# Performance work log

Hardware: AMD Instinct MI355X
Metric: run time of the kernel (lower is better)

The kernel has to match this reference:

```python
import jax, jax.numpy as jnp
import numpy as np
import math

B, S, D, H, L, K = 4, 2048, 256, 8, 2, 3  # batch, seq, dim, heads, MTA layers, conv kernel
HS = D // H
EPS = 1e-6


def layer_norm(x, g, b):
    m = jnp.mean(x, axis=-1, keepdims=True)
    v = jnp.mean((x - m) ** 2, axis=-1, keepdims=True)
    return (x - m) * jax.lax.rsqrt(v + EPS) * g + b


def temporal_encoder(x, W, b):
    # x: [B,S,D]; W: [L,K,D,D] (WIO), b: [L,D]. Stack of kernel-3 'SAME' Conv1d, GELU between.
    for i in range(L):
        x = jax.lax.conv_general_dilated(
            x, W[i], window_strides=(1,), padding=[(1, 1)],
            dimension_numbers=("NWC", "WIO", "NWC")) + b[i]
        if i < L - 1:
            x = jax.nn.gelu(x)
    return x


def setup_inputs() -> dict:
    key = jax.random.key(0)
    ks = jax.random.split(key, 10)
    w = lambda k, shape: jax.random.normal(k, shape, jnp.float32) * 0.02
    return {
        "x": jax.random.normal(ks[0], (B, S, D), jnp.float32),
        "ln1_g": jnp.ones((D,), jnp.float32), "ln1_b": jnp.zeros((D,), jnp.float32),
        "Wq": w(ks[1], (L, K, D, D)), "bq": jnp.zeros((L, D), jnp.float32),
        "Wk": w(ks[2], (L, K, D, D)), "bk": jnp.zeros((L, D), jnp.float32),
        "Wv": w(ks[3], (L, K, D, D)), "bv": jnp.zeros((L, D), jnp.float32),
        "ln2_g": jnp.ones((D,), jnp.float32), "ln2_b": jnp.zeros((D,), jnp.float32),
        "Wo1": w(ks[4], (D, D)), "bo1": jnp.zeros((D,), jnp.float32),
        "Wo2": w(ks[5], (D, D)), "bo2": jnp.zeros((D,), jnp.float32),
        "mask": jax.random.randint(ks[6], (B, S), 0, 2).astype(jnp.int32),
    }


def reference(x, ln1_g, ln1_b, Wq, bq, Wk, bk, Wv, bv, ln2_g, ln2_b, Wo1, bo1, Wo2, bo2, mask):
    b_, s_ = x.shape[0], x.shape[1]
    h = layer_norm(x, ln1_g, ln1_b)
    q = temporal_encoder(h, Wq, bq).reshape(b_, s_, H, HS)
    k = temporal_encoder(h, Wk, bk).reshape(b_, s_, H, HS)
    v = temporal_encoder(h, Wv, bv).reshape(b_, s_, H, HS)
    # attention scores [B,H,S,S]
    scores = jnp.einsum("bqhd,bkhd->bhqk", q, k) / math.sqrt(HS)
    m = mask[:, None, None, :].astype(scores.dtype)  # [B,1,1,S]
    scores = scores + (1.0 - m) * (-1e30)
    probs = jax.nn.softmax(scores, axis=-1)
    attn = jnp.einsum("bhqk,bkhd->bqhd", probs, v).reshape(b_, s_, D)
    residual = x + attn  # dropout p=0
    o = layer_norm(residual, ln2_g, ln2_b)
    o = jax.nn.gelu(o @ Wo1 + bo1)  # 1x1 Conv1D == per-token linear
    o = o @ Wo2 + bo2 + residual
    return o
```

## Files before the change

### kernel.cpp

```cpp
#include <hip/hip_runtime.h>
#include <hip/hip_bf16.h>
#include <math.h>

#define BB 4
#define SS 2048
#define DD 256
#define HH 8
#define HSZ 32

typedef __attribute__((ext_vector_type(8))) short short8;
typedef __attribute__((ext_vector_type(4))) float f32x4;

__device__ __forceinline__ void gload_lds16(const void* g, void* l) {
    __builtin_amdgcn_global_load_lds((const unsigned int*)g, (unsigned int*)l,
                                     16, 0, 0);
}

__device__ __forceinline__ float exp2_hw(float x) {
    float r;
    asm("v_exp_f32 %0, %1" : "=v"(r) : "v"(x));
    return r;
}

__device__ __forceinline__ unsigned int perm_pack(float a, float b, unsigned int sel) {
    unsigned int r;
    asm("v_perm_b32 %0, %1, %2, %3"
        : "=v"(r)
        : "v"(__float_as_uint(b)), "v"(__float_as_uint(a)), "s"(sel));
    return r;
}

__device__ __forceinline__ float gelu_f(float x) {
    float x3 = x * x * x;
    float z = 0.7978845608028654f * fmaf(0.044715f, x3, x);
    float e = __expf(2.0f * z);
    float t = 1.0f - 2.0f / (e + 1.0f);
    return 0.5f * x * (1.0f + t);
}

__device__ __forceinline__ unsigned short f2bf(float f) {
    unsigned int u = __float_as_uint(f);
    u = (u + 0x7fffu + ((u >> 16) & 1u)) >> 16;
    return (unsigned short)u;
}

template<bool HASRES>
__device__ __forceinline__ void ln_wave_body(
    int t, int lane,
    const float* __restrict__ x, const float* __restrict__ addin,
    const float* __restrict__ g, const float* __restrict__ bvec,
    float* __restrict__ resid_out, unsigned short* __restrict__ oln_bf)
{
    const int base = t * DD + lane * 4;
    float4 v4 = *(const float4*)&x[base];
    if (HASRES) {
        float4 a4 = *(const float4*)&addin[base];
        v4.x += a4.x; v4.y += a4.y; v4.z += a4.z; v4.w += a4.w;
        *(float4*)&resid_out[base] = v4;
    }
    float s = (v4.x + v4.y) + (v4.z + v4.w);
    #pragma unroll
    for (int o = 1; o < 64; o <<= 1) s += __shfl_xor(s, o);
    float mean = s * (1.0f / 256.0f);
    float dx = v4.x - mean, dy = v4.y - mean, dz = v4.z - mean, dw = v4.w - mean;
    float q = (dx * dx + dy * dy) + (dz * dz + dw * dw);
    #pragma unroll
    for (int o = 1; o < 64; o <<= 1) q += __shfl_xor(q, o);
    float r = rsqrtf(q * (1.0f / 256.0f) + 1e-6f);
    const float4 g4 = *(const float4*)&g[lane * 4];
    const float4 b4 = *(const float4*)&bvec[lane * 4];
    ushort4 o4;
    o4.x = f2bf(dx * r * g4.x + b4.x);
    o4.y = f2bf(dy * r * g4.y + b4.y);
    o4.z = f2bf(dz * r * g4.z + b4.z);
    o4.w = f2bf(dw * r * g4.w + b4.w);
    *(ushort4*)&oln_bf[base] = o4;
}

__global__ __launch_bounds__(256) void prep_kernel(
    const float* __restrict__ Wq, const float* __restrict__ Wk,
    const float* __restrict__ Wv, const float* __restrict__ Wo1,
    const float* __restrict__ Wo2, unsigned short* __restrict__ wt,
    const float* __restrict__ x, const float* __restrict__ ln1g,
    const float* __restrict__ ln1b, unsigned short* __restrict__ h_bf,
    const int* __restrict__ mask, float* __restrict__ maskf)
{
    if (blockIdx.x < 1280) {
        const int WCp = 3 * DD * DD;
        const int WMp = DD * DD;
        const float* src; unsigned short* dst; int R, rel;
        int i = blockIdx.x;
        if (i < 1152) {
            int seg = i / 192; rel = i % 192; R = 768;
            src = seg == 0 ? Wq : seg == 1 ? Wq + WCp : seg == 2 ? Wk :
                  seg == 3 ? Wk + WCp : seg == 4 ? Wv : Wv + WCp;
            dst = wt + (size_t)seg * WCp;
        } else {
            int j = i - 1152; int seg = j / 64; rel = j % 64; R = 256;
            src = seg == 0 ? Wo1 : Wo2;
            dst = wt + (size_t)6 * WCp + (size_t)seg * WMp;
        }
        __shared__ unsigned short t[32][33];
        const int tx = threadIdx.x & 31, ty = threadIdx.x >> 5;
        const int r0 = (rel / 8) * 32, c0 = (rel % 8) * 32;
        #pragma unroll
        for (int j = 0; j < 32; j += 8)
            t[ty + j][tx] = f2bf(src[(r0 + ty + j) * 256 + c0 + tx]);
        __syncthreads();
        #pragma unroll
        for (int j = 0; j < 32; j += 8)
            dst[(size_t)(c0 + ty + j) * R + r0 + tx] = t[tx][ty + j];
    } else if (blockIdx.x < 3328) {
        const int wv = threadIdx.x >> 6, lane = threadIdx.x & 63;
        ln_wave_body<false>((blockIdx.x - 1280) * 4 + wv, lane,
                            x, nullptr, ln1g, ln1b, nullptr, h_bf);
    } else {
        const float M_ON  = -8.0f * 1.4426950408889634f;
        const float M_OFF = -1.442695e30f;
        int i = (blockIdx.x - 3328) * 1024 + threadIdx.x * 4;
        int4 m4 = *(const int4*)&mask[i];
        float4 f4;
        f4.x = m4.x ? M_ON : M_OFF;
        f4.y = m4.y ? M_ON : M_OFF;
        f4.z = m4.z ? M_ON : M_OFF;
        f4.w = m4.w ? M_ON : M_OFF;
        *(float4*)&maskf[i] = f4;
    }
}

__global__ __launch_bounds__(256, 3) void convdual_kernel(
    const unsigned short* __restrict__ in,
    const unsigned short* __restrict__ W0a, const unsigned short* __restrict__ W0b,
    const unsigned short* __restrict__ W0c,
    const unsigned short* __restrict__ W1a, const unsigned short* __restrict__ W1b,
    const unsigned short* __restrict__ W1c,
    const float* __restrict__ ba, const float* __restrict__ bb,
    const float* __restrict__ bc,
    unsigned short* __restrict__ oQ, unsigned short* __restrict__ oK,
    unsigned short* __restrict__ oV, int S)
{
    constexpr int LDW = 264;
    __shared__ __align__(16) unsigned short stage[36 * LDW];
    __shared__ __align__(16) unsigned short wbuf[2][8192];

    unsigned short* const inter = stage;

    const int set = blockIdx.x % 3;
    const int tile = blockIdx.x / 3;
    const unsigned short* W0 = set == 0 ? W0a : (set == 1 ? W0b : W0c);
    const unsigned short* W1 = set == 0 ? W1a : (set == 1 ? W1b : W1c);
    const float* bias         = set == 0 ? ba  : (set == 1 ? bb  : bc);
    unsigned short* outp      = set == 0 ? oQ  : (set == 1 ? oK  : oV);

    const int tid = threadIdx.x;
    const int lane = tid & 63, wv = tid >> 6;
    const int lm = lane & 15, lq = lane >> 4;
    const int tpb = S / 32;
    const int b = tile / tpb;
    const int s0 = (tile % tpb) * 32;
    const int NC = S / 32;
    const int c = s0 >> 5;

    for (int i = tid; i < 36 * 32; i += 256) {
        int r = i >> 5, c8 = (i & 31) << 3;
        int s = s0 + r - 2;
        int4 val = make_int4(0, 0, 0, 0);
        if (s >= 0 && s < S)
            val = *(const int4*)&in[(size_t)(b * S + s) * 256 + c8];
        *(int4*)&stage[r * LDW + c8] = val;
    }

    const int n0 = wv * 64;

    const char* wsrc0[4];
    const char* wsrc1[4];
    char* wdst[4];
    {
        const unsigned int Lb = (unsigned int)(wv * 4096 + lane * 16);
        #pragma unroll
        for (int j = 0; j < 4; ++j) {
            unsigned int L = Lb + j * 1024u;
            unsigned int SL = L ^ (((L >> 7) & 7u) << 4);
            unsigned int so = (SL >> 6) * 1536u + (SL & 63u);
            wsrc0[j] = (const char*)W0 + so;
            wsrc1[j] = (const char*)W1 + so;
            wdst[j] = (char*)wbuf + (wv * 4096 + j * 1024);
        }
    }
    unsigned int boff[4];
    #pragma unroll
    for (int nt = 0; nt < 4; ++nt) {
        unsigned int och = (unsigned int)(n0 + nt * 16 + lm);
        unsigned int R = och * 64u + (unsigned int)lq * 16u;
        boff[nt] = R ^ (((R >> 7) & 7u) << 4);
    }

    __syncthreads();

    {
        f32x4 acc[3][4];
        #pragma unroll
        for (int mt = 0; mt < 3; ++mt)
            #pragma unroll
            for (int nt = 0; nt < 4; ++nt) acc[mt][nt] = (f32x4){0.f, 0.f, 0.f, 0.f};

        #pragma unroll
        for (int j = 0; j < 4; ++j) gload_lds16(wsrc0[j],      wdst[j]);
        #pragma unroll
        for (int j = 0; j < 4; ++j) gload_lds16(wsrc0[j] + 64, wdst[j] + 16384);

        short8 a0c, a1c, a2c;
        {
            const int icc0 = lq * 8;
            int r20 = 32 + lm; r20 = r20 > 35 ? 35 : r20;
            a0c = *(const short8*)&stage[lm * LDW + icc0];
            a1c = *(const short8*)&stage[(16 + lm) * LDW + icc0];
            a2c = *(const short8*)&stage[r20 * LDW + icc0];
        }

        asm volatile("s_waitcnt vmcnt(4)" ::: "memory");
        __builtin_amdgcn_sched_barrier(0);
        short8 bfc[4];
        #pragma unroll
        for (int nt = 0; nt < 4; ++nt)
            bfc[nt] = *(const short8*)((const char*)wbuf + boff[nt]);
        asm volatile("s_waitcnt lgkmcnt(0)" ::: "memory");
        __builtin_amdgcn_sched_barrier(0);

        #pragma unroll
        for (int it = 0; it < 24; ++it) {
            short8 bfn[4];
            short8 a0n, a1n, a2n;
            if (it + 1 < 24) {
                asm volatile("s_waitcnt vmcnt(0)" ::: "memory");
                __builtin_amdgcn_sched_barrier(0);
                const char* wb = (const char*)wbuf + (((it + 1) & 1) << 14);
                #pragma unroll
                for (int nt = 0; nt < 4; ++nt)
                    bfn[nt] = *(const short8*)(wb + boff[nt]);
                const int kk = (it + 1) >> 3;
                const int icc = ((it + 1) & 7) * 32 + lq * 8;
                int r2 = kk + 32 + lm; r2 = r2 > 35 ? 35 : r2;
                a0n = *(const short8*)&stage[(kk + lm) * LDW + icc];
                a1n = *(const short8*)&stage[(kk + 16 + lm) * LDW + icc];
                a2n = *(const short8*)&stage[r2 * LDW + icc];
            }
            if (it + 2 < 24) {
                char* ld = (char*)wbuf + ((it & 1) << 14);
                const int soff = (it + 2) * 64;
                #pragma unroll
                for (int j = 0; j < 4; ++j)
                    gload_lds16(wsrc0[j] + soff, ld + (wdst[j] - (char*)wbuf));
            }
            __builtin_amdgcn_s_setprio(1);
            #pragma unroll
            for (int nt = 0; nt < 4; ++nt) {
                acc[0][nt] = __builtin_amdgcn_mfma_f32_16x16x32_bf16(a0c, bfc[nt], acc[0][nt], 0, 0, 0);
                acc[1][nt] = __builtin_amdgcn_mfma_f32_16x16x32_bf16(a1c, bfc[nt], acc[1][nt], 0, 0, 0);
                acc[2][nt] = __builtin_amdgcn_mfma_f32_16x16x32_bf16(a2c, bfc[nt], acc[2][nt], 0, 0, 0);
            }
            __builtin_amdgcn_s_setprio(0);
            if (it + 1 < 24) {
                #pragma unroll
                for (int nt = 0; nt < 4; ++nt) bfc[nt] = bfn[nt];
                a0c = a0n; a1c = a1n; a2c = a2n;
            }
        }

        __syncthreads();

        #pragma unroll
        for (int j = 0; j < 4; ++j) gload_lds16(wsrc1[j],      wdst[j]);
        #pragma unroll
        for (int j = 0; j < 4; ++j) gload_lds16(wsrc1[j] + 64, wdst[j] + 16384);

        #pragma unroll
        for (int mt = 0; mt < 3; ++mt)
            #pragma unroll
            for (int nt = 0; nt < 4; ++nt) {
                int ch = n0 + nt * 16 + lm;
                float bv = bias[ch];
                #pragma unroll
                for (int r = 0; r < 4; ++r) {
                    int j = mt * 16 + lq * 4 + r;
                    if (j < 34) {
                        int token = s0 - 1 + j;
                        unsigned short v = (token >= 0 && token < S)
                            ? f2bf(gelu_f(acc[mt][nt][r] + bv)) : (unsigned short)0;
                        inter[j * LDW + ch] = v;
                    }
                }
            }
    }
    __syncthreads();

    f32x4 acc2[2][4];
    #pragma unroll
    for (int mt = 0; mt < 2; ++mt)
        #pragma unroll
        for (int nt = 0; nt < 4; ++nt) acc2[mt][nt] = (f32x4){0.f, 0.f, 0.f, 0.f};
    {
        short8 a0c, a1c;
        {
            const int icc0 = lq * 8;
            a0c = *(const short8*)&inter[lm * LDW + icc0];
            a1c = *(const short8*)&inter[(16 + lm) * LDW + icc0];
        }

        asm volatile("s_waitcnt vmcnt(4)" ::: "memory");
        __builtin_amdgcn_sched_barrier(0);
        short8 bfc[4];
        #pragma unroll
        for (int nt = 0; nt < 4; ++nt)
            bfc[nt] = *(const short8*)((const char*)wbuf + boff[nt]);
        asm volatile("s_waitcnt lgkmcnt(0)" ::: "memory");
        __builtin_amdgcn_sched_barrier(0);

        #pragma unroll
        for (int it = 0; it < 24; ++it) {
            short8 bfn[4];
            short8 a0n, a1n;
            if (it + 1 < 24) {
                asm volatile("s_waitcnt vmcnt(0)" ::: "memory");
                __builtin_amdgcn_sched_barrier(0);
                const char* wb = (const char*)wbuf + (((it + 1) & 1) << 14);
                #pragma unroll
                for (int nt = 0; nt < 4; ++nt)
                    bfn[nt] = *(const short8*)(wb + boff[nt]);
                const int kk = (it + 1) >> 3;
                const int icc = ((it + 1) & 7) * 32 + lq * 8;
                a0n = *(const short8*)&inter[(kk + lm) * LDW + icc];
                a1n = *(const short8*)&inter[(kk + 16 + lm) * LDW + icc];
            }
            if (it + 2 < 24) {
                char* ld = (char*)wbuf + ((it & 1) << 14);
                const int soff = (it + 2) * 64;
                #pragma unroll
                for (int j = 0; j < 4; ++j)
                    gload_lds16(wsrc1[j] + soff, ld + (wdst[j] - (char*)wbuf));
            }
            __builtin_amdgcn_s_setprio(1);
            #pragma unroll
            for (int nt = 0; nt < 4; ++nt) {
                acc2[0][nt] = __builtin_amdgcn_mfma_f32_16x16x32_bf16(a0c, bfc[nt], acc2[0][nt], 0, 0, 0);
                acc2[1][nt] = __builtin_amdgcn_mfma_f32_16x16x32_bf16(a1c, bfc[nt], acc2[1][nt], 0, 0, 0);
            }
            __builtin_amdgcn_s_setprio(0);
            if (it + 1 < 24) {
                #pragma unroll
                for (int nt = 0; nt < 4; ++nt) bfc[nt] = bfn[nt];
                a0c = a0n; a1c = a1n;
            }
        }
    }

    __syncthreads();
    if (set < 2) {
        #pragma unroll
        for (int mt = 0; mt < 2; ++mt)
            #pragma unroll
            for (int nt = 0; nt < 4; ++nt) {
                int o = n0 + nt * 16 + lm;
                int d = o & 31, h = o >> 5;
                float bv = bias[256 + o];
                #pragma unroll
                for (int r = 0; r < 4; ++r) {
                    int t = lq * 4 + r;
                    stage[mt * 4096 + (h * 64 + (d >> 3) * 16 + t) * 8 + (d & 7)] =
                        f2bf(acc2[mt][nt][r] + bv);
                }
            }
        __syncthreads();
        int h = tid >> 5;
        size_t base = ((size_t)(b * 8 + h) * NC + c) * 1024;
        #pragma unroll
        for (int half = 0; half < 2; ++half) {
            int4 v0 = *(const int4*)&stage[half * 4096 + tid * 16];
            int4 v1 = *(const int4*)&stage[half * 4096 + tid * 16 + 8];
            size_t dst = base + half * 512 + (tid & 31) * 16;
            *(int4*)&outp[dst] = v0;
            *(int4*)&outp[dst + 8] = v1;
        }
    } else {
        #pragma unroll
        for (int mt = 0; mt < 2; ++mt)
            #pragma unroll
            for (int nt = 0; nt < 4; ++nt) {
                int o = n0 + nt * 16 + lm;
                int d = o & 31, h = o >> 5;
                float bv = bias[256 + o];
                #pragma unroll
                for (int r = 0; r < 4; ++r) {
                    int t = lq * 4 + r;
                    stage[mt * 4096 +
                          ((h * 2 + (d >> 4)) * 32 + (t >> 3) * 16 + (d & 15)) * 8 + (t & 7)] =
                        f2bf(acc2[mt][nt][r] + bv);
                }
            }
        __syncthreads();
        int h = tid >> 5, dh = (tid >> 4) & 1;
        size_t base = ((size_t)(b * 8 + h) * NC + c) * 1024;
        #pragma unroll
        for (int half = 0; half < 2; ++half) {
            int4 v0 = *(const int4*)&stage[half * 4096 + tid * 16];
            int4 v1 = *(const int4*)&stage[half * 4096 + tid * 16 + 8];
            size_t dst = base + dh * 512 + half * 256 + (tid & 15) * 16;
            *(int4*)&outp[dst] = v0;
            *(int4*)&outp[dst + 8] = v1;
        }
    }
}

__global__ __launch_bounds__(256, 2) void tail_kernel(
    const float* __restrict__ x, const float* __restrict__ attn,
    const float* __restrict__ g2, const float* __restrict__ b2,
    const unsigned short* __restrict__ W1, const float* __restrict__ bo1,
    const unsigned short* __restrict__ W2, const float* __restrict__ bo2,
    float* __restrict__ out, int S)
{
    constexpr int LDW = 264;
    __shared__ __align__(16) unsigned short h_lds[16 * LDW];
    __shared__ __align__(16) unsigned short h2_lds[16 * LDW];
    __shared__ __align__(16) float resid_lds[16][DD];
    __shared__ __align__(16) unsigned short wbuf[2][8192];

    const int tid = threadIdx.x;
    const int lane = tid & 63, wv = tid >> 6;
    const int lm = lane & 15, lq = lane >> 4;
    const int t0 = blockIdx.x * 16;
    const int n0 = wv * 64;

    const char* wsrc1[4];
    const char* wsrc2[4];
    char* wdst[4];
    {
        const unsigned int Lb = (unsigned int)(wv * 4096 + lane * 16);
        #pragma unroll
        for (int j = 0; j < 4; ++j) {
            unsigned int L = Lb + j * 1024u;
            unsigned int SL = L ^ (((L >> 7) & 7u) << 4);
            unsigned int so = (SL >> 6) * 512u + (SL & 63u);
            wsrc1[j] = (const char*)W1 + so;
            wsrc2[j] = (const char*)W2 + so;
            wdst[j] = (char*)wbuf + (wv * 4096 + j * 1024);
        }
    }
    unsigned int boff[4];
    #pragma unroll
    for (int nt = 0; nt < 4; ++nt) {
        unsigned int och = (unsigned int)(n0 + nt * 16 + lm);
        unsigned int R = och * 64u + (unsigned int)lq * 16u;
        boff[nt] = R ^ (((R >> 7) & 7u) << 4);
    }

    #pragma unroll
    for (int j = 0; j < 4; ++j) gload_lds16(wsrc1[j],      wdst[j]);
    #pragma unroll
    for (int j = 0; j < 4; ++j) gload_lds16(wsrc1[j] + 64, wdst[j] + 16384);

    #pragma unroll
    for (int j = 0; j < 4; ++j) {
        int t = wv * 4 + j;
        int base = (t0 + t) * DD + lane * 4;
        float4 v4 = *(const float4*)&x[base];
        float4 a4 = *(const float4*)&attn[base];
        v4.x += a4.x; v4.y += a4.y; v4.z += a4.z; v4.w += a4.w;
        *(float4*)&resid_lds[t][lane * 4] = v4;
        float s = (v4.x + v4.y) + (v4.z + v4.w);
        #pragma unroll
        for (int o = 1; o < 64; o <<= 1) s += __shfl_xor(s, o);
        float mean = s * (1.0f / 256.0f);
        float dx = v4.x - mean, dy = v4.y - mean, dz = v4.z - mean, dw = v4.w - mean;
        float q = (dx * dx + dy * dy) + (dz * dz + dw * dw);
        #pragma unroll
        for (int o = 1; o < 64; o <<= 1) q += __shfl_xor(q, o);
        float r = rsqrtf(q * (1.0f / 256.0f) + 1e-6f);
        const float4 g4 = *(const float4*)&g2[lane * 4];
        const float4 b4 = *(const float4*)&b2[lane * 4];
        ushort4 o4;
        o4.x = f2bf(dx * r * g4.x + b4.x);
        o4.y = f2bf(dy * r * g4.y + b4.y);
        o4.z = f2bf(dz * r * g4.z + b4.z);
        o4.w = f2bf(dw * r * g4.w + b4.w);
        *(ushort4*)&h_lds[t * LDW + lane * 4] = o4;
    }
    __syncthreads();

    {
        f32x4 acc[4];
        #pragma unroll
        for (int nt = 0; nt < 4; ++nt) acc[nt] = (f32x4){0.f, 0.f, 0.f, 0.f};

        short8 a0c = *(const short8*)&h_lds[lm * LDW + lq * 8];
        asm volatile("s_waitcnt vmcnt(4)" ::: "memory");
        __builtin_amdgcn_sched_barrier(0);
        short8 bfc[4];
        #pragma unroll
        for (int nt = 0; nt < 4; ++nt)
            bfc[nt] = *(const short8*)((const char*)wbuf + boff[nt]);
        asm volatile("s_waitcnt lgkmcnt(0)" ::: "memory");
        __builtin_amdgcn_sched_barrier(0);

        #pragma unroll
        for (int it = 0; it < 8; ++it) {
            short8 bfn[4], a0n;
            if (it + 1 < 8) {
                asm volatile("s_waitcnt vmcnt(0)" ::: "memory");
                __builtin_amdgcn_sched_barrier(0);
                const char* wb = (const char*)wbuf + (((it + 1) & 1) << 14);
                #pragma unroll
                for (int nt = 0; nt < 4; ++nt)
                    bfn[nt] = *(const short8*)(wb + boff[nt]);
                a0n = *(const short8*)&h_lds[lm * LDW + (it + 1) * 32 + lq * 8];
            }
            if (it + 2 < 8) {
                char* ld = (char*)wbuf + ((it & 1) << 14);
                const int soff = (it + 2) * 64;
                #pragma unroll
                for (int j = 0; j < 4; ++j)
                    gload_lds16(wsrc1[j] + soff, ld + (wdst[j] - (char*)wbuf));
            }
            __builtin_amdgcn_s_setprio(1);
            #pragma unroll
            for (int nt = 0; nt < 4; ++nt)
                acc[nt] = __builtin_amdgcn_mfma_f32_16x16x32_bf16(a0c, bfc[nt], acc[nt], 0, 0, 0);
            __builtin_amdgcn_s_setprio(0);
            if (it + 1 < 8) {
                #pragma unroll
                for (int nt = 0; nt < 4; ++nt) bfc[nt] = bfn[nt];
                a0c = a0n;
            }
        }

        #pragma unroll
        for (int j = 0; j < 4; ++j) gload_lds16(wsrc2[j],      wdst[j]);
        #pragma unroll
        for (int j = 0; j < 4; ++j) gload_lds16(wsrc2[j] + 64, wdst[j] + 16384);

        #pragma unroll
        for (int nt = 0; nt < 4; ++nt) {
            int ch = n0 + nt * 16 + lm;
            float bv = bo1[ch];
            #pragma unroll
            for (int r = 0; r < 4; ++r) {
                int tok = lq * 4 + r;
                h2_lds[tok * LDW + ch] = f2bf(gelu_f(acc[nt][r] + bv));
            }
        }
    }
    __syncthreads();

    {
        f32x4 acc[4];
        #pragma unroll
        for (int nt = 0; nt < 4; ++nt) acc[nt] = (f32x4){0.f, 0.f, 0.f, 0.f};

        short8 a0c = *(const short8*)&h2_lds[lm * LDW + lq * 8];
        asm volatile("s_waitcnt vmcnt(4)" ::: "memory");
        __builtin_amdgcn_sched_barrier(0);
        short8 bfc[4];
        #pragma unroll
        for (int nt = 0; nt < 4; ++nt)
            bfc[nt] = *(const short8*)((const char*)wbuf + boff[nt]);
        asm volatile("s_waitcnt lgkmcnt(0)" ::: "memory");
        __builtin_amdgcn_sched_barrier(0);

        #pragma unroll
        for (int it = 0; it < 8; ++it) {
            short8 bfn[4], a0n;
            if (it + 1 < 8) {
                asm volatile("s_waitcnt vmcnt(0)" ::: "memory");
                __builtin_amdgcn_sched_barrier(0);
                const char* wb = (const char*)wbuf + (((it + 1) & 1) << 14);
                #pragma unroll
                for (int nt = 0; nt < 4; ++nt)
                    bfn[nt] = *(const short8*)(wb + boff[nt]);
                a0n = *(const short8*)&h2_lds[lm * LDW + (it + 1) * 32 + lq * 8];
            }
            if (it + 2 < 8) {
                char* ld = (char*)wbuf + ((it & 1) << 14);
                const int soff = (it + 2) * 64;
                #pragma unroll
                for (int j = 0; j < 4; ++j)
                    gload_lds16(wsrc2[j] + soff, ld + (wdst[j] - (char*)wbuf));
            }
            __builtin_amdgcn_s_setprio(1);
            #pragma unroll
            for (int nt = 0; nt < 4; ++nt)
                acc[nt] = __builtin_amdgcn_mfma_f32_16x16x32_bf16(a0c, bfc[nt], acc[nt], 0, 0, 0);
            __builtin_amdgcn_s_setprio(0);
            if (it + 1 < 8) {
                #pragma unroll
                for (int nt = 0; nt < 4; ++nt) bfc[nt] = bfn[nt];
                a0c = a0n;
            }
        }
        #pragma unroll
        for (int nt = 0; nt < 4; ++nt) {
            int ch = n0 + nt * 16 + lm;
            float bv = bo2[ch];
            #pragma unroll
            for (int r = 0; r < 4; ++r) {
                int tok = lq * 4 + r;
                out[(size_t)(t0 + tok) * DD + ch] = acc[nt][r] + bv + resid_lds[tok][ch];
            }
        }
    }
}

__global__ __launch_bounds__(256) void attn_mfma_kernel(
    const unsigned short* __restrict__ Qf, const unsigned short* __restrict__ Kf,
    const unsigned short* __restrict__ Vf, const float* __restrict__ maskf,
    float* __restrict__ Out, int S, int H)
{
    constexpr int LDP = 40;
    __shared__ __align__(16) unsigned short p_lds[4][16 * LDP];

    const int bh = ((blockIdx.x & 7) << 2) | ((blockIdx.x >> 3) & 3);
    const int qt = (blockIdx.x >> 5) * 64;
    const int b = bh / H;
    const int tid = threadIdx.x;
    const int lane = tid & 63, wv = tid >> 6;
    const int lm = lane & 15, lq = lane >> 4;
    const int q0 = qt + wv * 16;
    const int NC = S / 32;

    const size_t base = (size_t)bh * NC * 1024;
    short8 qfrag = *(const short8*)&Qf[base + (size_t)(q0 >> 5) * 1024
                                      + ((q0 >> 4) & 1) * 512 + lane * 8];
    const unsigned short* kp = Kf + base + lane * 8;
    const unsigned short* vp = Vf + base + lane * 8;

    short8 ones;
    #pragma unroll
    for (int j = 0; j < 8; ++j) ones[j] = (short)0x3F80;

    f32x4 o0 = {0.f, 0.f, 0.f, 0.f}, o1 = {0.f, 0.f, 0.f, 0.f};
    const f32x4 zf = {0.f, 0.f, 0.f, 0.f};
    float l[4] = {0.f, 0.f, 0.f, 0.f};

    const float scale2 = 0.17677669529663687f * 1.4426950408889634f;
    const unsigned int psel = 0x07060302u;
    const float* mp0 = maskf + b * S + lq * 4;
    const float* mp1 = mp0 + 16;

    unsigned short* pw = p_lds[wv];
    const int pst = lm * LDP + lq * 4;
    const int prd = lm * LDP + lq * 8;

    short8 k0c = *(const short8*)(kp);
    short8 k1c = *(const short8*)(kp + 512);
    short8 v0c = *(const short8*)(vp);
    short8 v1c = *(const short8*)(vp + 512);

    #pragma unroll 2
    for (int c = 0; c < NC; ++c) {
        int cn = c + 1 < NC ? c + 1 : c;
        short8 k0n = *(const short8*)(kp + (size_t)cn * 1024);
        short8 k1n = *(const short8*)(kp + (size_t)cn * 1024 + 512);
        short8 v0n = *(const short8*)(vp + (size_t)cn * 1024);
        short8 v1n = *(const short8*)(vp + (size_t)cn * 1024 + 512);

        f32x4 s0 = __builtin_amdgcn_mfma_f32_16x16x32_bf16(k0c, qfrag, zf, 0, 0, 0);
        f32x4 s1 = __builtin_amdgcn_mfma_f32_16x16x32_bf16(k1c, qfrag, zf, 0, 0, 0);

        float4 mf0 = *(const float4*)(mp0 + c * 32);
        float4 mf1 = *(const float4*)(mp1 + c * 32);

        float p[8];
        p[0] = exp2_hw(fmaf(s0[0], scale2, mf0.x));
        p[1] = exp2_hw(fmaf(s0[1], scale2, mf0.y));
        p[2] = exp2_hw(fmaf(s0[2], scale2, mf0.z));
        p[3] = exp2_hw(fmaf(s0[3], scale2, mf0.w));
        p[4] = exp2_hw(fmaf(s1[0], scale2, mf1.x));
        p[5] = exp2_hw(fmaf(s1[1], scale2, mf1.y));
        p[6] = exp2_hw(fmaf(s1[2], scale2, mf1.z));
        p[7] = exp2_hw(fmaf(s1[3], scale2, mf1.w));

        uint2 w0, w1;
        w0.x = perm_pack(p[0], p[1], psel); w0.y = perm_pack(p[2], p[3], psel);
        w1.x = perm_pack(p[4], p[5], psel); w1.y = perm_pack(p[6], p[7], psel);
        *(uint2*)&pw[pst] = w0;
        *(uint2*)&pw[pst + 16] = w1;

        short8 pA = *(const short8*)&pw[prd];

        f32x4 lf = __builtin_amdgcn_mfma_f32_16x16x32_bf16(pA, ones, zf, 0, 0, 0);
        o0 = __builtin_amdgcn_mfma_f32_16x16x32_bf16(pA, v0c, o0, 0, 0, 0);
        o1 = __builtin_amdgcn_mfma_f32_16x16x32_bf16(pA, v1c, o1, 0, 0, 0);
        #pragma unroll
        for (int r = 0; r < 4; ++r) l[r] += lf[r];

        k0c = k0n; k1c = k1n; v0c = v0n; v1c = v1n;
    }

    #pragma unroll
    for (int r = 0; r < 4; ++r) {
        float inv = 1.0f / l[r];
        size_t ob = (size_t)(b * S + q0 + lq * 4 + r) * 256 + (bh % H) * 32;
        Out[ob + lm] = o0[r] * inv;
        Out[ob + 16 + lm] = o1[r] * inv;
    }
}

extern "C" void kernel_launch(void* const* d_in, const int* in_sizes, int n_in,
                              void* d_out, int out_size, void* d_ws, size_t ws_size,
                              hipStream_t stream) {
    (void)in_sizes; (void)n_in; (void)out_size; (void)ws_size;
    const float* x    = (const float*)d_in[0];
    const float* ln1g = (const float*)d_in[1];
    const float* ln1b = (const float*)d_in[2];
    const float* Wq   = (const float*)d_in[3];
    const float* bq   = (const float*)d_in[4];
    const float* Wk   = (const float*)d_in[5];
    const float* bk   = (const float*)d_in[6];
    const float* Wv   = (const float*)d_in[7];
    const float* bv   = (const float*)d_in[8];
    const float* ln2g = (const float*)d_in[9];
    const float* ln2b = (const float*)d_in[10];
    const float* Wo1  = (const float*)d_in[11];
    const float* bo1  = (const float*)d_in[12];
    const float* Wo2  = (const float*)d_in[13];
    const float* bo2  = (const float*)d_in[14];
    const int*   mask = (const int*)d_in[15];
    float* out = (float*)d_out;

    const int S = SS, H = HH;
    const int T = BB * SS;
    const size_t NE = (size_t)T * DD;
    float* ws    = (float*)d_ws;
    float* attn  = ws + 0 * NE;
    float* maskf = ws + 1 * NE;
    unsigned short* qf_g  = (unsigned short*)(ws + 2 * NE);
    unsigned short* kf_g  = qf_g + NE;
    unsigned short* h_bf  = kf_g + NE;
    unsigned short* wt    = h_bf + NE;
    const int WC = 3 * DD * DD;
    const int WM = DD * DD;
    unsigned short* wtq0 = wt;
    unsigned short* wtq1 = wt + WC;
    unsigned short* wtk0 = wt + 2 * WC;
    unsigned short* wtk1 = wt + 3 * WC;
    unsigned short* wtv0 = wt + 4 * WC;
    unsigned short* wtv1 = wt + 5 * WC;
    unsigned short* wto1 = wt + 6 * WC;
    unsigned short* wto2 = wt + 6 * WC + WM;
    unsigned short* vf_g = wt + 6 * WC + 2 * WM;

    prep_kernel<<<1280 + T / 4 + 8, 256, 0, stream>>>(
        Wq, Wk, Wv, Wo1, Wo2, wt, x, ln1g, ln1b, h_bf, mask, maskf);

    convdual_kernel<<<(T / 32) * 3, 256, 0, stream>>>(
        h_bf, wtq0, wtk0, wtv0, wtq1, wtk1, wtv1, bq, bk, bv,
        qf_g, kf_g, vf_g, S);

    attn_mfma_kernel<<<BB * H * (S / 64), 256, 0, stream>>>(qf_g, kf_g, vf_g, maskf, attn, S, H);

    tail_kernel<<<T / 16, 256, 0, stream>>>(
        x, attn, ln2g, ln2b, wto1, bo1, wto2, bo2, out, S);
}
```

Measured before the change: 203.1 us.

## Pre-swizzle weights into K-chunk-major layout and deepen LDS prefetch pipeline

```diff
diff --git a/kernel.cpp b/kernel.cpp
--- a/kernel.cpp
+++ b/kernel.cpp
@@ -88,15 +88,15 @@
     if (blockIdx.x < 1280) {
         const int WCp = 3 * DD * DD;
         const int WMp = DD * DD;
-        const float* src; unsigned short* dst; int R, rel;
+        const float* src; unsigned short* dst; int rel;
         int i = blockIdx.x;
         if (i < 1152) {
-            int seg = i / 192; rel = i % 192; R = 768;
+            int seg = i / 192; rel = i % 192;
             src = seg == 0 ? Wq : seg == 1 ? Wq + WCp : seg == 2 ? Wk :
                   seg == 3 ? Wk + WCp : seg == 4 ? Wv : Wv + WCp;
             dst = wt + (size_t)seg * WCp;
         } else {
-            int j = i - 1152; int seg = j / 64; rel = j % 64; R = 256;
+            int j = i - 1152; int seg = j / 64; rel = j % 64;
             src = seg == 0 ? Wo1 : Wo2;
             dst = wt + (size_t)6 * WCp + (size_t)seg * WMp;
         }
@@ -108,8 +108,13 @@
             t[ty + j][tx] = f2bf(src[(r0 + ty + j) * 256 + c0 + tx]);
         __syncthreads();
         #pragma unroll
-        for (int j = 0; j < 32; j += 8)
-            dst[(size_t)(c0 + ty + j) * R + r0 + tx] = t[tx][ty + j];
+        for (int j = 0; j < 32; j += 8) {
+            unsigned int och = (unsigned int)(c0 + ty + j);
+            unsigned int k   = (unsigned int)(r0 + tx);
+            unsigned int u   = och * 32u + (k & 31u);
+            u ^= ((u >> 6) & 7u) << 3;
+            dst[(size_t)(k >> 5) * 8192 + u] = t[tx][ty + j];
+        }
     } else if (blockIdx.x < 3328) {
         const int wv = threadIdx.x >> 6, lane = threadIdx.x & 63;
         ln_wave_body<false>((blockIdx.x - 1280) * 4 + wv, lane,
@@ -172,21 +177,11 @@
 
     const int n0 = wv * 64;
 
-    const char* wsrc0[4];
-    const char* wsrc1[4];
-    char* wdst[4];
-    {
-        const unsigned int Lb = (unsigned int)(wv * 4096 + lane * 16);
-        #pragma unroll
-        for (int j = 0; j < 4; ++j) {
-            unsigned int L = Lb + j * 1024u;
-            unsigned int SL = L ^ (((L >> 7) & 7u) << 4);
-            unsigned int so = (SL >> 6) * 1536u + (SL & 63u);
-            wsrc0[j] = (const char*)W0 + so;
-            wsrc1[j] = (const char*)W1 + so;
-            wdst[j] = (char*)wbuf + (wv * 4096 + j * 1024);
-        }
-    }
+    const int wq = wv * 4096;
+    const char* w0p = (const char*)W0 + wq + lane * 16;
+    const char* w1p = (const char*)W1 + wq + lane * 16;
+    char* const wb0 = (char*)wbuf;
+
     unsigned int boff[4];
     #pragma unroll
     for (int nt = 0; nt < 4; ++nt) {
@@ -205,9 +200,9 @@
             for (int nt = 0; nt < 4; ++nt) acc[mt][nt] = (f32x4){0.f, 0.f, 0.f, 0.f};
 
         #pragma unroll
-        for (int j = 0; j < 4; ++j) gload_lds16(wsrc0[j],      wdst[j]);
-        #pragma unroll
-        for (int j = 0; j < 4; ++j) gload_lds16(wsrc0[j] + 64, wdst[j] + 16384);
+        for (int j = 0; j < 4; ++j) gload_lds16(w0p + j * 1024,         wb0 + wq + j * 1024);
+        #pragma unroll
+        for (int j = 0; j < 4; ++j) gload_lds16(w0p + 16384 + j * 1024, wb0 + 16384 + wq + j * 1024);
 
         short8 a0c, a1c, a2c;
         {
@@ -223,18 +218,28 @@
         short8 bfc[4];
         #pragma unroll
         for (int nt = 0; nt < 4; ++nt)
-            bfc[nt] = *(const short8*)((const char*)wbuf + boff[nt]);
-        asm volatile("s_waitcnt lgkmcnt(0)" ::: "memory");
-        __builtin_amdgcn_sched_barrier(0);
+            bfc[nt] = *(const short8*)(wb0 + boff[nt]);
 
         #pragma unroll
         for (int it = 0; it < 24; ++it) {
+            asm volatile("s_waitcnt lgkmcnt(0)" ::: "memory");
+            __builtin_amdgcn_sched_barrier(0);
+            if (it + 2 < 24) {
+                char* ld = wb0 + ((it & 1) << 14) + wq;
+                const int soff = (it + 2) * 16384;
+                #pragma unroll
+                for (int j = 0; j < 4; ++j)
+                    gload_lds16(w0p + soff + j * 1024, ld + j * 1024);
+            }
+            __builtin_amdgcn_sched_barrier(0);
+            if (it < 22)       { asm volatile("s_waitcnt vmcnt(4)" ::: "memory"); }
+            else if (it == 22) { asm volatile("s_waitcnt vmcnt(0)" ::: "memory"); }
+            __builtin_amdgcn_sched_barrier(0);
+
             short8 bfn[4];
             short8 a0n, a1n, a2n;
             if (it + 1 < 24) {
-                asm volatile("s_waitcnt vmcnt(0)" ::: "memory");
-                __builtin_amdgcn_sched_barrier(0);
-                const char* wb = (const char*)wbuf + (((it + 1) & 1) << 14);
+                const char* wb = wb0 + (((it + 1) & 1) << 14);
                 #pragma unroll
                 for (int nt = 0; nt < 4; ++nt)
                     bfn[nt] = *(const short8*)(wb + boff[nt]);
@@ -245,13 +250,6 @@
                 a1n = *(const short8*)&stage[(kk + 16 + lm) * LDW + icc];
                 a2n = *(const short8*)&stage[r2 * LDW + icc];
             }
-            if (it + 2 < 24) {
-                char* ld = (char*)wbuf + ((it & 1) << 14);
-                const int soff = (it + 2) * 64;
-                #pragma unroll
-                for (int j = 0; j < 4; ++j)
-                    gload_lds16(wsrc0[j] + soff, ld + (wdst[j] - (char*)wbuf));
-            }
             __builtin_amdgcn_s_setprio(1);
             #pragma unroll
             for (int nt = 0; nt < 4; ++nt) {
@@ -270,9 +268,9 @@
         __syncthreads();
 
         #pragma unroll
-        for (int j = 0; j < 4; ++j) gload_lds16(wsrc1[j],      wdst[j]);
-        #pragma unroll
-        for (int j = 0; j < 4; ++j) gload_lds16(wsrc1[j] + 64, wdst[j] + 16384);
+        for (int j = 0; j < 4; ++j) gload_lds16(w1p + j * 1024,         wb0 + wq + j * 1024);
+        #pragma unroll
+        for (int j = 0; j < 4; ++j) gload_lds16(w1p + 16384 + j * 1024, wb0 + 16384 + wq + j * 1024);
 
         #pragma unroll
         for (int mt = 0; mt < 3; ++mt)
@@ -300,6 +298,7 @@
         #pragma unroll
         for (int nt = 0; nt < 4; ++nt) acc2[mt][nt] = (f32x4){0.f, 0.f, 0.f, 0.f};
     {
+        char* const wb0 = (char*)wbuf;
         short8 a0c, a1c;
         {
             const int icc0 = lq * 8;
@@ -312,18 +311,28 @@
         short8 bfc[4];
         #pragma unroll
         for (int nt = 0; nt < 4; ++nt)
-            bfc[nt] = *(const short8*)((const char*)wbuf + boff[nt]);
-        asm volatile("s_waitcnt lgkmcnt(0)" ::: "memory");
-        __builtin_amdgcn_sched_barrier(0);
+            bfc[nt] = *(const short8*)(wb0 + boff[nt]);
 
         #pragma unroll
         for (int it = 0; it < 24; ++it) {
+            asm volatile("s_waitcnt lgkmcnt(0)" ::: "memory");
+            __builtin_amdgcn_sched_barrier(0);
+            if (it + 2 < 24) {
+                char* ld = wb0 + ((it & 1) << 14) + wq;
+                const int soff = (it + 2) * 16384;
+                #pragma unroll
+                for (int j = 0; j < 4; ++j)
+                    gload_lds16(w1p + soff + j * 1024, ld + j * 1024);
+            }
+            __builtin_amdgcn_sched_barrier(0);
+            if (it < 22)       { asm volatile("s_waitcnt vmcnt(4)" ::: "memory"); }
+            else if (it == 22) { asm volatile("s_waitcnt vmcnt(0)" ::: "memory"); }
+            __builtin_amdgcn_sched_barrier(0);
+
             short8 bfn[4];
             short8 a0n, a1n;
             if (it + 1 < 24) {
-                asm volatile("s_waitcnt vmcnt(0)" ::: "memory");
-                __builtin_amdgcn_sched_barrier(0);
-                const char* wb = (const char*)wbuf + (((it + 1) & 1) << 14);
+                const char* wb = wb0 + (((it + 1) & 1) << 14);
                 #pragma unroll
                 for (int nt = 0; nt < 4; ++nt)
                     bfn[nt] = *(const short8*)(wb + boff[nt]);
@@ -331,13 +340,6 @@
                 const int icc = ((it + 1) & 7) * 32 + lq * 8;
                 a0n = *(const short8*)&inter[(kk + lm) * LDW + icc];
                 a1n = *(const short8*)&inter[(kk + 16 + lm) * LDW + icc];
-            }
-            if (it + 2 < 24) {
-                char* ld = (char*)wbuf + ((it & 1) << 14);
-                const int soff = (it + 2) * 64;
-                #pragma unroll
-                for (int j = 0; j < 4; ++j)
-                    gload_lds16(wsrc1[j] + soff, ld + (wdst[j] - (char*)wbuf));
             }
             __builtin_amdgcn_s_setprio(1);
             #pragma unroll
@@ -430,21 +432,11 @@
     const int t0 = blockIdx.x * 16;
     const int n0 = wv * 64;
 
-    const char* wsrc1[4];
-    const char* wsrc2[4];
-    char* wdst[4];
-    {
-        const unsigned int Lb = (unsigned int)(wv * 4096 + lane * 16);
-        #pragma unroll
-        for (int j = 0; j < 4; ++j) {
-            unsigned int L = Lb + j * 1024u;
-            unsigned int SL = L ^ (((L >> 7) & 7u) << 4);
-            unsigned int so = (SL >> 6) * 512u + (SL & 63u);
-            wsrc1[j] = (const char*)W1 + so;
-            wsrc2[j] = (const char*)W2 + so;
-            wdst[j] = (char*)wbuf + (wv * 4096 + j * 1024);
-        }
-    }
+    const int wq = wv * 4096;
+    const char* w1p = (const char*)W1 + wq + lane * 16;
+    const char* w2p = (const char*)W2 + wq + lane * 16;
+    char* const wb0 = (char*)wbuf;
+
     unsigned int boff[4];
     #pragma unroll
     for (int nt = 0; nt < 4; ++nt) {
@@ -454,9 +446,9 @@
     }
 
     #pragma unroll
-    for (int j = 0; j < 4; ++j) gload_lds16(wsrc1[j],      wdst[j]);
-    #pragma unroll
-    for (int j = 0; j < 4; ++j) gload_lds16(wsrc1[j] + 64, wdst[j] + 16384);
+    for (int j = 0; j < 4; ++j) gload_lds16(w1p + j * 1024,         wb0 + wq + j * 1024);
+    #pragma unroll
+    for (int j = 0; j < 4; ++j) gload_lds16(w1p + 16384 + j * 1024, wb0 + 16384 + wq + j * 1024);
 
     #pragma unroll
     for (int j = 0; j < 4; ++j) {
@@ -497,28 +489,31 @@
         short8 bfc[4];
         #pragma unroll
         for (int nt = 0; nt < 4; ++nt)
-            bfc[nt] = *(const short8*)((const char*)wbuf + boff[nt]);
-        asm volatile("s_waitcnt lgkmcnt(0)" ::: "memory");
-        __builtin_amdgcn_sched_barrier(0);
+            bfc[nt] = *(const short8*)(wb0 + boff[nt]);
 
         #pragma unroll
         for (int it = 0; it < 8; ++it) {
+            asm volatile("s_waitcnt lgkmcnt(0)" ::: "memory");
+            __builtin_amdgcn_sched_barrier(0);
+            if (it + 2 < 8) {
+                char* ld = wb0 + ((it & 1) << 14) + wq;
+                const int soff = (it + 2) * 16384;
+                #pragma unroll
+                for (int j = 0; j < 4; ++j)
+                    gload_lds16(w1p + soff + j * 1024, ld + j * 1024);
+            }
+            __builtin_amdgcn_sched_barrier(0);
+            if (it < 6)       { asm volatile("s_waitcnt vmcnt(4)" ::: "memory"); }
+            else if (it == 6) { asm volatile("s_waitcnt vmcnt(0)" ::: "memory"); }
+            __builtin_amdgcn_sched_barrier(0);
+
             short8 bfn[4], a0n;
             if (it + 1 < 8) {
-                asm volatile("s_waitcnt vmcnt(0)" ::: "memory");
-                __builtin_amdgcn_sched_barrier(0);
-                const char* wb = (const char*)wbuf + (((it + 1) & 1) << 14);
+                const char* wb = wb0 + (((it + 1) & 1) << 14);
                 #pragma unroll
                 for (int nt = 0; nt < 4; ++nt)
                     bfn[nt] = *(const short8*)(wb + boff[nt]);
                 a0n = *(const short8*)&h_lds[lm * LDW + (it + 1) * 32 + lq * 8];
-            }
-            if (it + 2 < 8) {
-                char* ld = (char*)wbuf + ((it & 1) << 14);
-                const int soff = (it + 2) * 64;
-                #pragma unroll
-                for (int j = 0; j < 4; ++j)
-                    gload_lds16(wsrc1[j] + soff, ld + (wdst[j] - (char*)wbuf));
             }
             __builtin_amdgcn_s_setprio(1);
             #pragma unroll
@@ -532,10 +527,12 @@
             }
         }
 
-        #pragma unroll
-        for (int j = 0; j < 4; ++j) gload_lds16(wsrc2[j],      wdst[j]);
-        #pragma unroll
-        for (int j = 0; j < 4; ++j) gload_lds16(wsrc2[j] + 64, wdst[j] + 16384);
+        asm volatile("s_waitcnt lgkmcnt(0)" ::: "memory");
+        __builtin_amdgcn_sched_barrier(0);
+        #pragma unroll
+        for (int j = 0; j < 4; ++j) gload_lds16(w2p + j * 1024,         wb0 + wq + j * 1024);
+        #pragma unroll
+        for (int j = 0; j < 4; ++j) gload_lds16(w2p + 16384 + j * 1024, wb0 + 16384 + wq + j * 1024);
 
         #pragma unroll
         for (int nt = 0; nt < 4; ++nt) {
@@ -561,28 +558,31 @@
         short8 bfc[4];
         #pragma unroll
         for (int nt = 0; nt < 4; ++nt)
-            bfc[nt] = *(const short8*)((const char*)wbuf + boff[nt]);
-        asm volatile("s_waitcnt lgkmcnt(0)" ::: "memory");
-        __builtin_amdgcn_sched_barrier(0);
+            bfc[nt] = *(const short8*)(wb0 + boff[nt]);
 
         #pragma unroll
         for (int it = 0; it < 8; ++it) {
+            asm volatile("s_waitcnt lgkmcnt(0)" ::: "memory");
+            __builtin_amdgcn_sched_barrier(0);
+            if (it + 2 < 8) {
+                char* ld = wb0 + ((it & 1) << 14) + wq;
+                const int soff = (it + 2) * 16384;
+                #pragma unroll
+                for (int j = 0; j < 4; ++j)
+                    gload_lds16(w2p + soff + j * 1024, ld + j * 1024);
+            }
+            __builtin_amdgcn_sched_barrier(0);
+            if (it < 6)       { asm volatile("s_waitcnt vmcnt(4)" ::: "memory"); }
+            else if (it == 6) { asm volatile("s_waitcnt vmcnt(0)" ::: "memory"); }
+            __builtin_amdgcn_sched_barrier(0);
+
             short8 bfn[4], a0n;
             if (it + 1 < 8) {
-                asm volatile("s_waitcnt vmcnt(0)" ::: "memory");
-                __builtin_amdgcn_sched_barrier(0);
-                const char* wb = (const char*)wbuf + (((it + 1) & 1) << 14);
+                const char* wb = wb0 + (((it + 1) & 1) << 14);
                 #pragma unroll
                 for (int nt = 0; nt < 4; ++nt)
                     bfn[nt] = *(const short8*)(wb + boff[nt]);
                 a0n = *(const short8*)&h2_lds[lm * LDW + (it + 1) * 32 + lq * 8];
-            }
-            if (it + 2 < 8) {
-                char* ld = (char*)wbuf + ((it & 1) << 14);
-                const int soff = (it + 2) * 64;
-                #pragma unroll
-                for (int j = 0; j < 4; ++j)
-                    gload_lds16(wsrc2[j] + soff, ld + (wdst[j] - (char*)wbuf));
             }
             __builtin_amdgcn_s_setprio(1);
             #pragma unroll
```

Result: faster. 189.5 us (-6.7%).
